# Performance work log

Hardware: AMD Instinct MI355X
Metric: run time of the kernel (lower is better)

## Reference

```python
import jax, jax.numpy as jnp
import numpy as np

D_MODEL = 1024
N_EXPERTS = 8
TOP_K = 2
B, S = 2, 2048


def setup_inputs() -> dict:
    key = jax.random.key(0)
    ks = jax.random.split(key, 12)
    d, e, h = D_MODEL, N_EXPERTS, 4 * D_MODEL
    sd = 1.0 / np.sqrt(d)
    sh = 1.0 / np.sqrt(h)
    return {
        "x": jax.random.normal(ks[0], (B, S, d), dtype=jnp.float32),
        "noise": jax.random.uniform(ks[1], (B, S, e), dtype=jnp.float32),
        # router linear [d, E]
        "Wr": jax.random.uniform(ks[2], (d, e), minval=-sd, maxval=sd),
        "br": jax.random.uniform(ks[3], (e,), minval=-sd, maxval=sd),
        # noise linear [d, E]
        "Wn": jax.random.uniform(ks[4], (d, e), minval=-sd, maxval=sd),
        "bn": jax.random.uniform(ks[5], (e,), minval=-sd, maxval=sd),
        # stacked expert FFN weights
        "W1": jax.random.uniform(ks[6], (e, d, h), minval=-sd, maxval=sd),
        "b1": jax.random.uniform(ks[7], (e, h), minval=-sd, maxval=sd),
        "W2": jax.random.uniform(ks[8], (e, h, d), minval=-sh, maxval=sh),
        "b2": jax.random.uniform(ks[9], (e, d), minval=-sh, maxval=sh),
    }


def _moe_forward(x, noise, Wr, br, Wn, bn, W1, b1, W2, b2):
    e = Wr.shape[-1]
    # noisy top-k router
    logits = x @ Wr + br + jax.nn.softplus(x @ Wn + bn) * noise  # [B,S,E]
    top_v, top_i = jax.lax.top_k(logits, TOP_K)                  # [B,S,K]
    # softmax over sparse top-k (non-topk entries are -inf -> weight 0)
    gates_k = jax.nn.softmax(top_v, axis=-1)                     # [B,S,K]
    gating = jnp.sum(jax.nn.one_hot(top_i, e, dtype=x.dtype) * gates_k[..., None], axis=-2)  # [B,S,E]
    # experts (dropout in eval mode = identity). Non-selected experts have
    # gate 0, so the dense weighted sum equals the masked gather/scatter.
    hdn = jax.nn.relu(jnp.einsum('bsd,edh->bseh', x, W1) + b1)   # [B,S,E,4d]
    y = jnp.einsum('bseh,ehd->bsed', hdn, W2) + b2               # [B,S,E,d]
    return jnp.einsum('bse,bsed->bsd', gating, y)


def reference(x, noise, Wr, br, Wn, bn, W1, b1, W2, b2):
    return _moe_forward(x, noise, Wr, br, Wn, bn, W1, b1, W2, b2)
```

## Files before the change

### kernel.cpp

```cpp
#include <hip/hip_runtime.h>
#include <hip/hip_bf16.h>
#include <cstdint>
#include <cstddef>

#define D_MODEL 1024
#define N_EXP   8
#define HID     4096
#define T_TOK   4096
#define NPAIR   (T_TOK * 2)

#define WS_COUNTS   0
#define WS_CURSOR   32
#define WS_OFFSETS  64
#define WS_TOKE     128
#define WS_TOKG     32896
#define WS_LTOK     65664
#define WS_LGATE    98432
#define WS_XB       131328
#define WS_WB       (WS_XB + 8388608)
#define WS_H        (WS_WB + 67108864)

typedef __attribute__((ext_vector_type(8))) short bf16x8;
typedef __attribute__((ext_vector_type(4))) float f32x4;

__device__ __forceinline__ unsigned short f2bf(float f) {
    unsigned u = __float_as_uint(f);
    u += 0x7FFFu + ((u >> 16) & 1u);
    return (unsigned short)(u >> 16);
}

__device__ __forceinline__ void glds16(const void* g, void* l) {
    __builtin_amdgcn_global_load_lds(
        (const __attribute__((address_space(1))) void*)g,
        (__attribute__((address_space(3))) void*)l, 16, 0, 0);
}

__global__ __launch_bounds__(256) void k_router(
    const float* __restrict__ x, const float* __restrict__ noise,
    const float* __restrict__ Wr, const float* __restrict__ br,
    const float* __restrict__ Wn, const float* __restrict__ bn,
    int* __restrict__ counts, int* __restrict__ tok_e, float* __restrict__ tok_g)
{
    const int t   = blockIdx.x;
    const int tid = threadIdx.x;
    const int e   = tid & 7;
    const int g   = tid >> 3;
    const float* xr = x + (size_t)t * D_MODEL;

    float ar = 0.f, an = 0.f;
    const int ibase = g * 32;
    #pragma unroll 8
    for (int j = 0; j < 32; ++j) {
        const int i = ibase + j;
        const float xv = xr[i];
        ar = fmaf(xv, Wr[i * 8 + e], ar);
        an = fmaf(xv, Wn[i * 8 + e], an);
    }

    __shared__ float sR[256], sN[256];
    sR[tid] = ar; sN[tid] = an;
    __syncthreads();
    for (int off = 128; off >= 8; off >>= 1) {
        if (tid < off) { sR[tid] += sR[tid + off]; sN[tid] += sN[tid + off]; }
        __syncthreads();
    }

    __shared__ float lg[8];
    if (tid < 8) {
        const float z  = sN[tid] + bn[tid];
        const float sp = fmaxf(z, 0.f) + log1pf(expf(-fabsf(z)));
        lg[tid] = sR[tid] + br[tid] + sp * noise[t * 8 + tid];
    }
    __syncthreads();

    if (tid == 0) {
        float v0 = -INFINITY, v1 = -INFINITY;
        int   i0 = 0,         i1 = 0;
        #pragma unroll
        for (int ee = 0; ee < 8; ++ee) {
            const float v = lg[ee];
            if (v > v0)      { v1 = v0; i1 = i0; v0 = v; i0 = ee; }
            else if (v > v1) { v1 = v;  i1 = ee; }
        }
        const float ew  = expf(v1 - v0);
        const float inv = 1.f / (1.f + ew);
        tok_e[t * 2 + 0] = i0;
        tok_e[t * 2 + 1] = i1;
        tok_g[t * 2 + 0] = inv;
        tok_g[t * 2 + 1] = ew * inv;
        atomicAdd(&counts[i0], 1);
        atomicAdd(&counts[i1], 1);
    }
}

__global__ void k_prefix(const int* __restrict__ counts, int* __restrict__ offsets)
{
    if (threadIdx.x == 0 && blockIdx.x == 0) {
        int acc = 0;
        #pragma unroll
        for (int e = 0; e < N_EXP; ++e) { offsets[e] = acc; acc += counts[e]; }
    }
}

__global__ __launch_bounds__(256) void k_scatter(
    const int* __restrict__ tok_e, const float* __restrict__ tok_g,
    const int* __restrict__ offsets, int* __restrict__ cursor,
    int* __restrict__ list_tok, float* __restrict__ list_gate)
{
    const int gid = blockIdx.x * 256 + threadIdx.x;
    if (gid >= NPAIR) return;
    const int e = tok_e[gid];
    const int p = atomicAdd(&cursor[e], 1);
    const int slot = offsets[e] + p;
    list_tok[slot]  = gid >> 1;
    list_gate[slot] = tok_g[gid];
}

__global__ __launch_bounds__(256) void k_cvt_x(
    const float* __restrict__ in, unsigned short* __restrict__ outp)
{
    const int i = (blockIdx.x * 256 + threadIdx.x) * 4;
    const float4 v = *(const float4*)(in + i);
    ushort4 o;
    o.x = f2bf(v.x); o.y = f2bf(v.y); o.z = f2bf(v.z); o.w = f2bf(v.w);
    *(ushort4*)(outp + i) = o;
}

__global__ __launch_bounds__(256) void k_cvtT(
    const float* __restrict__ in, unsigned short* __restrict__ outp, int R, int C)
{
    const size_t esz = (size_t)R * C;
    const float* ine = in + (size_t)blockIdx.z * esz;
    unsigned short* oute = outp + (size_t)blockIdx.z * esz;
    const int c0 = blockIdx.x * 32, r0 = blockIdx.y * 32;

    __shared__ float s[32][36];
    const int tid = threadIdx.x;
    const int lr = tid >> 3, lc = (tid & 7) * 4;
    const float4 v = *(const float4*)(ine + (size_t)(r0 + lr) * C + c0 + lc);
    s[lr][lc + 0] = v.x; s[lr][lc + 1] = v.y; s[lr][lc + 2] = v.z; s[lr][lc + 3] = v.w;
    __syncthreads();
    const int oc = tid >> 3, orp = (tid & 7) * 4;
    ushort4 o;
    o.x = f2bf(s[orp + 0][oc]); o.y = f2bf(s[orp + 1][oc]);
    o.z = f2bf(s[orp + 2][oc]); o.w = f2bf(s[orp + 3][oc]);
    *(ushort4*)(oute + (size_t)(c0 + oc) * R + r0 + orp) = o;
}

__global__ __launch_bounds__(256) void k_ffn1(
    const unsigned short* __restrict__ xb,
    const unsigned short* __restrict__ W1t,
    const float* __restrict__ b1,
    const int* __restrict__ counts, const int* __restrict__ offsets,
    const int* __restrict__ list_tok,
    unsigned short* __restrict__ H)
{
    const int e   = blockIdx.z;
    const int cnt = counts[e];
    const int m0  = blockIdx.y * 128;
    if (m0 >= cnt) return;
    const int base = offsets[e];
    const int n0   = blockIdx.x * 128;
    const unsigned short* __restrict__ Be = W1t + (size_t)e * (HID * D_MODEL);

    __shared__ __align__(16) unsigned short As[128 * 32];
    __shared__ __align__(16) unsigned short Bs[128 * 32];
    __shared__ int stok[128];

    const int tid = threadIdx.x;
    if (tid < 128) stok[tid] = list_tok[base + min(m0 + tid, cnt - 1)];
    __syncthreads();

    const int arow  = tid >> 2;
    const int kpart = (tid & 3) * 8;
    const size_t srcA0 = (size_t)stok[arow]      * D_MODEL + kpart;
    const size_t srcA1 = (size_t)stok[arow + 64] * D_MODEL + kpart;
    const size_t srcB0 = (size_t)(n0 + arow)      * D_MODEL + kpart;
    const size_t srcB1 = (size_t)(n0 + arow + 64) * D_MODEL + kpart;

    const int lane = tid & 63, lr = lane & 15, hk = lane >> 4;
    const int w = tid >> 6, wm = w >> 1, wn = w & 1;
    const int aoff = (wm * 64 + lr) * 32 + hk * 8;
    const int boff = (wn * 64 + lr) * 32 + hk * 8;

    f32x4 acc[4][4] = {};

    for (int kt = 0; kt < D_MODEL; kt += 32) {
        __syncthreads();
        glds16(xb + srcA0 + kt, (char*)As + tid * 16);
        glds16(xb + srcA1 + kt, (char*)As + (tid + 256) * 16);
        glds16(Be + srcB0 + kt, (char*)Bs + tid * 16);
        glds16(Be + srcB1 + kt, (char*)Bs + (tid + 256) * 16);
        __syncthreads();

        bf16x8 a[4], b[4];
        #pragma unroll
        for (int i = 0; i < 4; ++i) a[i] = *(const bf16x8*)(As + aoff + i * 16 * 32);
        #pragma unroll
        for (int j = 0; j < 4; ++j) b[j] = *(const bf16x8*)(Bs + boff + j * 16 * 32);
        #pragma unroll
        for (int i = 0; i < 4; ++i)
            #pragma unroll
            for (int j = 0; j < 4; ++j)
                acc[i][j] = __builtin_amdgcn_mfma_f32_16x16x32_bf16(a[i], b[j], acc[i][j], 0, 0, 0);
    }

    float bias[4];
    #pragma unroll
    for (int j = 0; j < 4; ++j) bias[j] = b1[(size_t)e * HID + n0 + wn * 64 + j * 16 + lr];

    #pragma unroll
    for (int i = 0; i < 4; ++i) {
        #pragma unroll
        for (int g = 0; g < 4; ++g) {
            const int m = m0 + wm * 64 + i * 16 + hk * 4 + g;
            if (m < cnt) {
                unsigned short* dst = H + (size_t)(base + m) * HID + n0 + wn * 64 + lr;
                #pragma unroll
                for (int j = 0; j < 4; ++j)
                    dst[j * 16] = f2bf(fmaxf(acc[i][j][g] + bias[j], 0.f));
            }
        }
    }
}

__global__ __launch_bounds__(256) void k_ffn2(
    const unsigned short* __restrict__ Hb,
    const unsigned short* __restrict__ W2t,
    const float* __restrict__ b2,
    const int* __restrict__ counts, const int* __restrict__ offsets,
    const int* __restrict__ list_tok, const float* __restrict__ list_gate,
    float* __restrict__ out)
{
    const int e   = blockIdx.z;
    const int cnt = counts[e];
    const int m0  = blockIdx.y * 128;
    if (m0 >= cnt) return;
    const int base = offsets[e];
    const int n0   = blockIdx.x * 128;
    const unsigned short* __restrict__ Be = W2t + (size_t)e * (D_MODEL * HID);

    __shared__ __align__(16) unsigned short As[128 * 32];
    __shared__ __align__(16) unsigned short Bs[128 * 32];

    const int tid  = threadIdx.x;
    const int arow = tid >> 2;
    const int kpart = (tid & 3) * 8;
    const size_t srcA0 = (size_t)(base + min(m0 + arow,      cnt - 1)) * HID + kpart;
    const size_t srcA1 = (size_t)(base + min(m0 + arow + 64, cnt - 1)) * HID + kpart;
    const size_t srcB0 = (size_t)(n0 + arow)      * HID + kpart;
    const size_t srcB1 = (size_t)(n0 + arow + 64) * HID + kpart;

    const int lane = tid & 63, lr = lane & 15, hk = lane >> 4;
    const int w = tid >> 6, wm = w >> 1, wn = w & 1;
    const int aoff = (wm * 64 + lr) * 32 + hk * 8;
    const int boff = (wn * 64 + lr) * 32 + hk * 8;

    f32x4 acc[4][4] = {};

    for (int kt = 0; kt < HID; kt += 32) {
        __syncthreads();
        glds16(Hb + srcA0 + kt, (char*)As + tid * 16);
        glds16(Hb + srcA1 + kt, (char*)As + (tid + 256) * 16);
        glds16(Be + srcB0 + kt, (char*)Bs + tid * 16);
        glds16(Be + srcB1 + kt, (char*)Bs + (tid + 256) * 16);
        __syncthreads();

        bf16x8 a[4], b[4];
        #pragma unroll
        for (int i = 0; i < 4; ++i) a[i] = *(const bf16x8*)(As + aoff + i * 16 * 32);
        #pragma unroll
        for (int j = 0; j < 4; ++j) b[j] = *(const bf16x8*)(Bs + boff + j * 16 * 32);
        #pragma unroll
        for (int i = 0; i < 4; ++i)
            #pragma unroll
            for (int j = 0; j < 4; ++j)
                acc[i][j] = __builtin_amdgcn_mfma_f32_16x16x32_bf16(a[i], b[j], acc[i][j], 0, 0, 0);
    }

    float bias[4];
    #pragma unroll
    for (int j = 0; j < 4; ++j) bias[j] = b2[(size_t)e * D_MODEL + n0 + wn * 64 + j * 16 + lr];

    #pragma unroll
    for (int i = 0; i < 4; ++i) {
        #pragma unroll
        for (int g = 0; g < 4; ++g) {
            const int m = m0 + wm * 64 + i * 16 + hk * 4 + g;
            if (m < cnt) {
                const int sl = base + m;
                const int tk = list_tok[sl];
                const float gt = list_gate[sl];
                float* dst = out + (size_t)tk * D_MODEL + n0 + wn * 64 + lr;
                #pragma unroll
                for (int j = 0; j < 4; ++j)
                    unsafeAtomicAdd(dst + j * 16, gt * (acc[i][j][g] + bias[j]));
            }
        }
    }
}

extern "C" void kernel_launch(void* const* d_in, const int* in_sizes, int n_in,
                              void* d_out, int out_size, void* d_ws, size_t ws_size,
                              hipStream_t stream)
{
    const float* x     = (const float*)d_in[0];
    const float* noise = (const float*)d_in[1];
    const float* Wr    = (const float*)d_in[2];
    const float* br    = (const float*)d_in[3];
    const float* Wn    = (const float*)d_in[4];
    const float* bn    = (const float*)d_in[5];
    const float* W1    = (const float*)d_in[6];
    const float* b1    = (const float*)d_in[7];
    const float* W2    = (const float*)d_in[8];
    const float* b2    = (const float*)d_in[9];
    float* out = (float*)d_out;

    char* ws = (char*)d_ws;
    int*   counts    = (int*)(ws + WS_COUNTS);
    int*   cursor    = (int*)(ws + WS_CURSOR);
    int*   offsets   = (int*)(ws + WS_OFFSETS);
    int*   tok_e     = (int*)(ws + WS_TOKE);
    float* tok_g     = (float*)(ws + WS_TOKG);
    int*   list_tok  = (int*)(ws + WS_LTOK);
    float* list_gate = (float*)(ws + WS_LGATE);
    unsigned short* xb = (unsigned short*)(ws + WS_XB);
    unsigned short* Wb = (unsigned short*)(ws + WS_WB);
    unsigned short* Hb = (unsigned short*)(ws + WS_H);

    hipMemsetAsync(ws, 0, 128, stream);
    hipMemsetAsync(d_out, 0, (size_t)out_size * sizeof(float), stream);

    k_cvt_x<<<T_TOK * D_MODEL / 1024, 256, 0, stream>>>(x, xb);
    k_cvtT<<<dim3(HID / 32, D_MODEL / 32, N_EXP), 256, 0, stream>>>(W1, Wb, D_MODEL, HID);
    k_router<<<T_TOK, 256, 0, stream>>>(x, noise, Wr, br, Wn, bn, counts, tok_e, tok_g);
    k_prefix<<<1, 64, 0, stream>>>(counts, offsets);
    k_scatter<<<NPAIR / 256, 256, 0, stream>>>(tok_e, tok_g, offsets, cursor,
                                               list_tok, list_gate);

    k_ffn1<<<dim3(HID / 128, NPAIR / 128, N_EXP), 256, 0, stream>>>(
        xb, Wb, b1, counts, offsets, list_tok, Hb);

    k_cvtT<<<dim3(D_MODEL / 32, HID / 32, N_EXP), 256, 0, stream>>>(W2, Wb, HID, D_MODEL);
    k_ffn2<<<dim3(D_MODEL / 128, NPAIR / 128, N_EXP), 256, 0, stream>>>(
        Hb, Wb, b2, counts, offsets, list_tok, list_gate, out);
}
```

Baseline: 460.6 us.

## Triple-buffer LDS in expert GEMMs with swizzled layout and remapped block order

Both expert FFN GEMMs now use a three-stage LDS ring filled by global_load_lds two tiles ahead, waiting with explicit vmcnt and a single barrier per k-step instead of two synchronisations around an unpipelined load. The LDS tile layout is XOR-swizzled so the fragment reads avoid bank conflicts. The grid is flattened and remapped so consecutive blocks spread across XCDs, with occupancy hints of 2 blocks per CU. FFN2 also caches token ids and gates in shared memory for the atomic epilogue. This raises LDS use and depends on hand-tuned waitcnt and barrier ordering.

Measured after the change: 466.6 us. About the same (+1.3%).

```diff
diff --git a/kernel.cpp b/kernel.cpp
--- a/kernel.cpp
+++ b/kernel.cpp
@@ -22,17 +22,24 @@
 
 typedef __attribute__((ext_vector_type(8))) short bf16x8;
 typedef __attribute__((ext_vector_type(4))) float f32x4;
-
-__device__ __forceinline__ unsigned short f2bf(float f) {
+typedef unsigned short u16;
+
+__device__ __forceinline__ u16 f2bf(float f) {
     unsigned u = __float_as_uint(f);
     u += 0x7FFFu + ((u >> 16) & 1u);
-    return (unsigned short)(u >> 16);
+    return (u16)(u >> 16);
 }
 
 __device__ __forceinline__ void glds16(const void* g, void* l) {
     __builtin_amdgcn_global_load_lds(
         (const __attribute__((address_space(1))) void*)g,
         (__attribute__((address_space(3))) void*)l, 16, 0, 0);
+}
+
+__device__ __forceinline__ void chunk_map(int c, int& row, int& kc) {
+    const int line = c >> 3, c8 = c & 7, u = c8 ^ (line & 7);
+    row = line * 2 + (u >> 2);
+    kc  = (u & 3) * 8;
 }
 
 __global__ __launch_bounds__(256) void k_router(
@@ -117,7 +124,7 @@
 }
 
 __global__ __launch_bounds__(256) void k_cvt_x(
-    const float* __restrict__ in, unsigned short* __restrict__ outp)
+    const float* __restrict__ in, u16* __restrict__ outp)
 {
     const int i = (blockIdx.x * 256 + threadIdx.x) * 4;
     const float4 v = *(const float4*)(in + i);
@@ -127,11 +134,11 @@
 }
 
 __global__ __launch_bounds__(256) void k_cvtT(
-    const float* __restrict__ in, unsigned short* __restrict__ outp, int R, int C)
+    const float* __restrict__ in, u16* __restrict__ outp, int R, int C)
 {
     const size_t esz = (size_t)R * C;
     const float* ine = in + (size_t)blockIdx.z * esz;
-    unsigned short* oute = outp + (size_t)blockIdx.z * esz;
+    u16* oute = outp + (size_t)blockIdx.z * esz;
     const int c0 = blockIdx.x * 32, r0 = blockIdx.y * 32;
 
     __shared__ float s[32][36];
@@ -147,67 +154,94 @@
     *(ushort4*)(oute + (size_t)(c0 + oc) * R + r0 + orp) = o;
 }
 
-__global__ __launch_bounds__(256) void k_ffn1(
-    const unsigned short* __restrict__ xb,
-    const unsigned short* __restrict__ W1t,
+__global__ __launch_bounds__(256, 2) void k_ffn1(
+    const u16* __restrict__ xb,
+    const u16* __restrict__ W1t,
     const float* __restrict__ b1,
     const int* __restrict__ counts, const int* __restrict__ offsets,
     const int* __restrict__ list_tok,
-    unsigned short* __restrict__ H)
-{
-    const int e   = blockIdx.z;
+    u16* __restrict__ H)
+{
+    const int bid = blockIdx.x;
+    const int e   = bid >> 11;
+    const int r   = bid & 2047;
+    const int wg  = ((r & 7) << 8) + (r >> 3);
+    const int n_t = wg >> 6;
+    const int m_t = wg & 63;
+
     const int cnt = counts[e];
-    const int m0  = blockIdx.y * 128;
+    const int m0  = m_t * 128;
     if (m0 >= cnt) return;
     const int base = offsets[e];
-    const int n0   = blockIdx.x * 128;
-    const unsigned short* __restrict__ Be = W1t + (size_t)e * (HID * D_MODEL);
-
-    __shared__ __align__(16) unsigned short As[128 * 32];
-    __shared__ __align__(16) unsigned short Bs[128 * 32];
+    const int n0   = n_t * 128;
+    const u16* __restrict__ Be = W1t + (size_t)e * (HID * D_MODEL);
+
+    __shared__ __align__(16) u16 SA[3 * 4096];
+    __shared__ __align__(16) u16 SB[3 * 4096];
     __shared__ int stok[128];
 
     const int tid = threadIdx.x;
     if (tid < 128) stok[tid] = list_tok[base + min(m0 + tid, cnt - 1)];
     __syncthreads();
 
-    const int arow  = tid >> 2;
-    const int kpart = (tid & 3) * 8;
-    const size_t srcA0 = (size_t)stok[arow]      * D_MODEL + kpart;
-    const size_t srcA1 = (size_t)stok[arow + 64] * D_MODEL + kpart;
-    const size_t srcB0 = (size_t)(n0 + arow)      * D_MODEL + kpart;
-    const size_t srcB1 = (size_t)(n0 + arow + 64) * D_MODEL + kpart;
+    int ar0, ak0, ar1, ak1;
+    chunk_map(tid, ar0, ak0);
+    chunk_map(tid + 256, ar1, ak1);
+    const u16* Asrc0 = xb + (size_t)stok[ar0] * D_MODEL + ak0;
+    const u16* Asrc1 = xb + (size_t)stok[ar1] * D_MODEL + ak1;
+    const u16* Bsrc0 = Be + (size_t)(n0 + ar0) * D_MODEL + ak0;
+    const u16* Bsrc1 = Be + (size_t)(n0 + ar1) * D_MODEL + ak1;
 
     const int lane = tid & 63, lr = lane & 15, hk = lane >> 4;
     const int w = tid >> 6, wm = w >> 1, wn = w & 1;
-    const int aoff = (wm * 64 + lr) * 32 + hk * 8;
-    const int boff = (wn * 64 + lr) * 32 + hk * 8;
+    const int colb  = ((((lr & 1) << 2) + hk) ^ (lr >> 1)) << 4;
+    const int baseA = ((wm * 32 + (lr >> 1)) << 7) + colb;
+    const int baseB = ((wn * 32 + (lr >> 1)) << 7) + colb;
+
+    float bias[4];
+    #pragma unroll
+    for (int j = 0; j < 4; ++j) bias[j] = b1[(size_t)e * HID + n0 + wn * 64 + j * 16 + lr];
 
     f32x4 acc[4][4] = {};
 
-    for (int kt = 0; kt < D_MODEL; kt += 32) {
-        __syncthreads();
-        glds16(xb + srcA0 + kt, (char*)As + tid * 16);
-        glds16(xb + srcA1 + kt, (char*)As + (tid + 256) * 16);
-        glds16(Be + srcB0 + kt, (char*)Bs + tid * 16);
-        glds16(Be + srcB1 + kt, (char*)Bs + (tid + 256) * 16);
-        __syncthreads();
-
+    auto STAGE = [&](int s, int t) {
+        const int kt = t * 32;
+        char* Ab = (char*)SA + s * 8192;
+        char* Bb = (char*)SB + s * 8192;
+        glds16(Asrc0 + kt, Ab + tid * 16);
+        glds16(Asrc1 + kt, Ab + (tid + 256) * 16);
+        glds16(Bsrc0 + kt, Bb + tid * 16);
+        glds16(Bsrc1 + kt, Bb + (tid + 256) * 16);
+    };
+    auto COMPUTE = [&](int s) {
+        const char* Ab = (const char*)SA + s * 8192;
+        const char* Bb = (const char*)SB + s * 8192;
         bf16x8 a[4], b[4];
         #pragma unroll
-        for (int i = 0; i < 4; ++i) a[i] = *(const bf16x8*)(As + aoff + i * 16 * 32);
-        #pragma unroll
-        for (int j = 0; j < 4; ++j) b[j] = *(const bf16x8*)(Bs + boff + j * 16 * 32);
+        for (int i = 0; i < 4; ++i) a[i] = *(const bf16x8*)(Ab + baseA + i * 1024);
+        #pragma unroll
+        for (int j = 0; j < 4; ++j) b[j] = *(const bf16x8*)(Bb + baseB + j * 1024);
         #pragma unroll
         for (int i = 0; i < 4; ++i)
             #pragma unroll
             for (int j = 0; j < 4; ++j)
                 acc[i][j] = __builtin_amdgcn_mfma_f32_16x16x32_bf16(a[i], b[j], acc[i][j], 0, 0, 0);
-    }
-
-    float bias[4];
-    #pragma unroll
-    for (int j = 0; j < 4; ++j) bias[j] = b1[(size_t)e * HID + n0 + wn * 64 + j * 16 + lr];
+    };
+
+    const int NT = D_MODEL / 32;
+    STAGE(0, 0);
+    STAGE(1, 1);
+    int sc = 0;
+    for (int t = 0; t < NT; ++t) {
+        if (t == NT - 1) { asm volatile("s_waitcnt vmcnt(0)" ::: "memory"); }
+        else             { asm volatile("s_waitcnt vmcnt(4)" ::: "memory"); }
+        __builtin_amdgcn_s_barrier();
+        __builtin_amdgcn_sched_barrier(0);
+        if (t + 2 < NT) { int ss = sc + 2; if (ss >= 3) ss -= 3; STAGE(ss, t + 2); }
+        __builtin_amdgcn_sched_barrier(0);
+        COMPUTE(sc);
+        if (++sc == 3) sc = 0;
+    }
 
     #pragma unroll
     for (int i = 0; i < 4; ++i) {
@@ -215,7 +249,7 @@
         for (int g = 0; g < 4; ++g) {
             const int m = m0 + wm * 64 + i * 16 + hk * 4 + g;
             if (m < cnt) {
-                unsigned short* dst = H + (size_t)(base + m) * HID + n0 + wn * 64 + lr;
+                u16* dst = H + (size_t)(base + m) * HID + n0 + wn * 64 + lr;
                 #pragma unroll
                 for (int j = 0; j < 4; ++j)
                     dst[j * 16] = f2bf(fmaxf(acc[i][j][g] + bias[j], 0.f));
@@ -224,63 +258,99 @@
     }
 }
 
-__global__ __launch_bounds__(256) void k_ffn2(
-    const unsigned short* __restrict__ Hb,
-    const unsigned short* __restrict__ W2t,
+__global__ __launch_bounds__(256, 2) void k_ffn2(
+    const u16* __restrict__ Hb,
+    const u16* __restrict__ W2t,
     const float* __restrict__ b2,
     const int* __restrict__ counts, const int* __restrict__ offsets,
     const int* __restrict__ list_tok, const float* __restrict__ list_gate,
     float* __restrict__ out)
 {
-    const int e   = blockIdx.z;
+    const int bid = blockIdx.x;
+    const int e   = bid >> 9;
+    const int r   = bid & 511;
+    const int wg  = ((r & 7) << 6) + (r >> 3);
+    const int n_t = wg >> 6;
+    const int m_t = wg & 63;
+
     const int cnt = counts[e];
-    const int m0  = blockIdx.y * 128;
+    const int m0  = m_t * 128;
     if (m0 >= cnt) return;
     const int base = offsets[e];
-    const int n0   = blockIdx.x * 128;
-    const unsigned short* __restrict__ Be = W2t + (size_t)e * (D_MODEL * HID);
-
-    __shared__ __align__(16) unsigned short As[128 * 32];
-    __shared__ __align__(16) unsigned short Bs[128 * 32];
-
-    const int tid  = threadIdx.x;
-    const int arow = tid >> 2;
-    const int kpart = (tid & 3) * 8;
-    const size_t srcA0 = (size_t)(base + min(m0 + arow,      cnt - 1)) * HID + kpart;
-    const size_t srcA1 = (size_t)(base + min(m0 + arow + 64, cnt - 1)) * HID + kpart;
-    const size_t srcB0 = (size_t)(n0 + arow)      * HID + kpart;
-    const size_t srcB1 = (size_t)(n0 + arow + 64) * HID + kpart;
+    const int n0   = n_t * 128;
+    const u16* __restrict__ Be = W2t + (size_t)e * (D_MODEL * HID);
+
+    __shared__ __align__(16) u16 SA[3 * 4096];
+    __shared__ __align__(16) u16 SB[3 * 4096];
+    __shared__ int   s_tok[128];
+    __shared__ float s_gate[128];
+
+    const int tid = threadIdx.x;
+    if (tid < 128) {
+        const int sl = base + min(m0 + tid, cnt - 1);
+        s_tok[tid]  = list_tok[sl];
+        s_gate[tid] = list_gate[sl];
+    }
+    __syncthreads();
+
+    int ar0, ak0, ar1, ak1;
+    chunk_map(tid, ar0, ak0);
+    chunk_map(tid + 256, ar1, ak1);
+    const u16* Asrc0 = Hb + (size_t)(base + min(m0 + ar0, cnt - 1)) * HID + ak0;
+    const u16* Asrc1 = Hb + (size_t)(base + min(m0 + ar1, cnt - 1)) * HID + ak1;
+    const u16* Bsrc0 = Be + (size_t)(n0 + ar0) * HID + ak0;
+    const u16* Bsrc1 = Be + (size_t)(n0 + ar1) * HID + ak1;
 
     const int lane = tid & 63, lr = lane & 15, hk = lane >> 4;
     const int w = tid >> 6, wm = w >> 1, wn = w & 1;
-    const int aoff = (wm * 64 + lr) * 32 + hk * 8;
-    const int boff = (wn * 64 + lr) * 32 + hk * 8;
+    const int colb  = ((((lr & 1) << 2) + hk) ^ (lr >> 1)) << 4;
+    const int baseA = ((wm * 32 + (lr >> 1)) << 7) + colb;
+    const int baseB = ((wn * 32 + (lr >> 1)) << 7) + colb;
+
+    float bias[4];
+    #pragma unroll
+    for (int j = 0; j < 4; ++j) bias[j] = b2[(size_t)e * D_MODEL + n0 + wn * 64 + j * 16 + lr];
 
     f32x4 acc[4][4] = {};
 
-    for (int kt = 0; kt < HID; kt += 32) {
-        __syncthreads();
-        glds16(Hb + srcA0 + kt, (char*)As + tid * 16);
-        glds16(Hb + srcA1 + kt, (char*)As + (tid + 256) * 16);
-        glds16(Be + srcB0 + kt, (char*)Bs + tid * 16);
-        glds16(Be + srcB1 + kt, (char*)Bs + (tid + 256) * 16);
-        __syncthreads();
-
+    auto STAGE = [&](int s, int t) {
+        const int kt = t * 32;
+        char* Ab = (char*)SA + s * 8192;
+        char* Bb = (char*)SB + s * 8192;
+        glds16(Asrc0 + kt, Ab + tid * 16);
+        glds16(Asrc1 + kt, Ab + (tid + 256) * 16);
+        glds16(Bsrc0 + kt, Bb + tid * 16);
+        glds16(Bsrc1 + kt, Bb + (tid + 256) * 16);
+    };
+    auto COMPUTE = [&](int s) {
+        const char* Ab = (const char*)SA + s * 8192;
+        const char* Bb = (const char*)SB + s * 8192;
         bf16x8 a[4], b[4];
         #pragma unroll
-        for (int i = 0; i < 4; ++i) a[i] = *(const bf16x8*)(As + aoff + i * 16 * 32);
-        #pragma unroll
-        for (int j = 0; j < 4; ++j) b[j] = *(const bf16x8*)(Bs + boff + j * 16 * 32);
+        for (int i = 0; i < 4; ++i) a[i] = *(const bf16x8*)(Ab + baseA + i * 1024);
+        #pragma unroll
+        for (int j = 0; j < 4; ++j) b[j] = *(const bf16x8*)(Bb + baseB + j * 1024);
         #pragma unroll
         for (int i = 0; i < 4; ++i)
             #pragma unroll
             for (int j = 0; j < 4; ++j)
                 acc[i][j] = __builtin_amdgcn_mfma_f32_16x16x32_bf16(a[i], b[j], acc[i][j], 0, 0, 0);
-    }
-
-    float bias[4];
-    #pragma unroll
-    for (int j = 0; j < 4; ++j) bias[j] = b2[(size_t)e * D_MODEL + n0 + wn * 64 + j * 16 + lr];
+    };
+
+    const int NT = HID / 32;
+    STAGE(0, 0);
+    STAGE(1, 1);
+    int sc = 0;
+    for (int t = 0; t < NT; ++t) {
+        if (t == NT - 1) { asm volatile("s_waitcnt vmcnt(0)" ::: "memory"); }
+        else             { asm volatile("s_waitcnt vmcnt(4)" ::: "memory"); }
+        __builtin_amdgcn_s_barrier();
+        __builtin_amdgcn_sched_barrier(0);
+        if (t + 2 < NT) { int ss = sc + 2; if (ss >= 3) ss -= 3; STAGE(ss, t + 2); }
+        __builtin_amdgcn_sched_barrier(0);
+        COMPUTE(sc);
+        if (++sc == 3) sc = 0;
+    }
 
     #pragma unroll
     for (int i = 0; i < 4; ++i) {
@@ -288,9 +358,9 @@
         for (int g = 0; g < 4; ++g) {
             const int m = m0 + wm * 64 + i * 16 + hk * 4 + g;
             if (m < cnt) {
-                const int sl = base + m;
-                const int tk = list_tok[sl];
-                const float gt = list_gate[sl];
+                const int   mm = m - m0;
+                const int   tk = s_tok[mm];
+                const float gt = s_gate[mm];
                 float* dst = out + (size_t)tk * D_MODEL + n0 + wn * 64 + lr;
                 #pragma unroll
                 for (int j = 0; j < 4; ++j)
@@ -324,9 +394,9 @@
     float* tok_g     = (float*)(ws + WS_TOKG);
     int*   list_tok  = (int*)(ws + WS_LTOK);
     float* list_gate = (float*)(ws + WS_LGATE);
-    unsigned short* xb = (unsigned short*)(ws + WS_XB);
-    unsigned short* Wb = (unsigned short*)(ws + WS_WB);
-    unsigned short* Hb = (unsigned short*)(ws + WS_H);
+    u16*   xb        = (u16*)(ws + WS_XB);
+    u16*   Wb        = (u16*)(ws + WS_WB);
+    u16*   Hb        = (u16*)(ws + WS_H);
 
     hipMemsetAsync(ws, 0, 128, stream);
     hipMemsetAsync(d_out, 0, (size_t)out_size * sizeof(float), stream);
@@ -338,10 +408,10 @@
     k_scatter<<<NPAIR / 256, 256, 0, stream>>>(tok_e, tok_g, offsets, cursor,
                                                list_tok, list_gate);
 
-    k_ffn1<<<dim3(HID / 128, NPAIR / 128, N_EXP), 256, 0, stream>>>(
-        xb, Wb, b1, counts, offsets, list_tok, Hb);
+    k_ffn1<<<N_EXP * 32 * 64, 256, 0, stream>>>(xb, Wb, b1, counts, offsets,
+                                                list_tok, Hb);
 
     k_cvtT<<<dim3(D_MODEL / 32, HID / 32, N_EXP), 256, 0, stream>>>(W2, Wb, HID, D_MODEL);
-    k_ffn2<<<dim3(D_MODEL / 128, NPAIR / 128, N_EXP), 256, 0, stream>>>(
-        Hb, Wb, b2, counts, offsets, list_tok, list_gate, out);
-}
+    k_ffn2<<<N_EXP * 8 * 64, 256, 0, stream>>>(Hb, Wb, b2, counts, offsets,
+                                               list_tok, list_gate, out);
+}
```
